# Kernel tuning notes

Hardware: AMD Instinct MI355X
Metric: run time of the kernel (lower is better)

The kernel has to match this reference:

```python
import jax, jax.numpy as jnp
import numpy as np

H_DIM = 1024
N_HEADS = 16
HEAD_D = H_DIM // N_HEADS  # 64


def setup_inputs() -> dict:
    key = jax.random.key(0)
    ks = jax.random.split(key, 10)
    B, T, C = 2, 2048, H_DIM
    init = 1.0 / np.sqrt(C)  # lecun_normal-scale stand-in
    src = jax.random.normal(ks[0], (B, T, C), dtype=jnp.float32)
    mask = jnp.ones((B, T), dtype=jnp.float32)  # unused when causal
    Wq = jax.random.normal(ks[1], (C, H_DIM), dtype=jnp.float32) * init
    Wk = jax.random.normal(ks[2], (C, H_DIM), dtype=jnp.float32) * init
    Wv = jax.random.normal(ks[3], (C, H_DIM), dtype=jnp.float32) * init
    Wo = jax.random.normal(ks[4], (H_DIM, H_DIM), dtype=jnp.float32) * init
    bq = jnp.zeros((H_DIM,), jnp.float32)
    bk = jnp.zeros((H_DIM,), jnp.float32)
    bv = jnp.zeros((H_DIM,), jnp.float32)
    bo = jnp.zeros((H_DIM,), jnp.float32)
    return {"src": src, "mask": mask, "Wq": Wq, "bq": bq, "Wk": Wk, "bk": bk,
            "Wv": Wv, "bv": bv, "Wo": Wo, "bo": bo}


def reference(src, mask, Wq, bq, Wk, bk, Wv, bv, Wo, bo):
    # MaskedCausalAttention forward, deterministic=True (dropout = identity),
    # use_causal_mask=True.
    B, T, C = src.shape
    N, D = N_HEADS, HEAD_D
    # q,k,v: [B, N, T, D]
    q = (src @ Wq + bq).reshape(B, T, N, D).transpose(0, 2, 1, 3)
    k = (src @ Wk + bk).reshape(B, T, N, D).transpose(0, 2, 1, 3)
    v = (src @ Wv + bv).reshape(B, T, N, D).transpose(0, 2, 1, 3)
    # scores: [B, N, T, T]
    scores = jnp.einsum('bntd,bnsd->bnts', q, k) / jnp.sqrt(jnp.float32(D))
    causal = jnp.tril(jnp.ones((T, T), dtype=bool))[None, None]
    scores = jnp.where(causal, scores, -jnp.inf)
    probs = jax.nn.softmax(scores, axis=-1)
    attn = jnp.einsum('bnts,bnsd->bntd', probs, v)  # [B, N, T, D]
    attn = attn.transpose(0, 2, 1, 3).reshape(B, T, N * D)
    return attn @ Wo + bo
```

## Files before the change

kernel.cpp:

```cpp
#include <hip/hip_runtime.h>
#include <hip/hip_bf16.h>

typedef __hip_bfloat16 bf16;
typedef __attribute__((ext_vector_type(8))) short short8;
typedef __attribute__((ext_vector_type(4))) float f32x4;

#define BATCH 2
#define SEQ   2048
#define HDIM  1024
#define NHEAD 16
#define DHEAD 64
#define MROWS (BATCH*SEQ)

#define QSCALE 0.18033688f
#define EXP2F(x) __builtin_amdgcn_exp2f(x)

static __device__ __forceinline__ short f2bs(float x) {
    __hip_bfloat16 h = (__hip_bfloat16)x;
    return *reinterpret_cast<short*>(&h);
}
static __device__ __forceinline__ unsigned int pk2(float a, float b) {
    __hip_bfloat162 h = __float22bfloat162_rn(make_float2(a, b));
    return *reinterpret_cast<unsigned int*>(&h);
}

static __device__ __forceinline__ void gload16(const void* g, void* l) {
    __builtin_amdgcn_global_load_lds(
        (const __attribute__((address_space(1))) unsigned int*)g,
        (__attribute__((address_space(3))) unsigned int*)l, 16, 0, 0);
}

__global__ __launch_bounds__(256) void prep1(const float* __restrict__ src,
        const float* __restrict__ Wq, const float* __restrict__ Wk,
        const float* __restrict__ Wv, const float* __restrict__ Wo,
        short* __restrict__ Sb, short* __restrict__ WT,
        short* __restrict__ WoT)
{
    __shared__ float t[64][65];
    const int bx = blockIdx.x, tid = threadIdx.x;
    if (bx < 4096) {
        int i = bx * 256 + tid;
        float4 v = ((const float4*)src)[i];
        ushort4 o;
        o.x = (unsigned short)f2bs(v.x);
        o.y = (unsigned short)f2bs(v.y);
        o.z = (unsigned short)f2bs(v.z);
        o.w = (unsigned short)f2bs(v.w);
        ((ushort4*)Sb)[i] = o;
        return;
    }
    const int tb = bx - 4096;
    const int wsel = tb >> 8;
    const float* W = (wsel == 0) ? Wq : (wsel == 1) ? Wk : (wsel == 2) ? Wv : Wo;
    short* dst = (wsel < 3) ? WT : WoT;
    const int roff = (wsel < 3) ? wsel * 1024 : 0;
    const int t8 = tb & 255;
    const int n0 = (t8 & 15) * 64, k0 = (t8 >> 4) * 64;
#pragma unroll
    for (int i = 0; i < 16; i++) {
        int idx = tid + i * 256, r = idx >> 6, c = idx & 63;
        t[r][c] = W[(size_t)(k0 + r) * HDIM + n0 + c];
    }
    __syncthreads();
#pragma unroll
    for (int i = 0; i < 16; i++) {
        int idx = tid + i * 256, c = idx >> 6, r = idx & 63;
        dst[(size_t)(roff + n0 + c) * HDIM + k0 + r] = f2bs(t[r][c]);
    }
}

__global__ __launch_bounds__(512, 2) void gemm_qkv(const short* __restrict__ A,
        const short* __restrict__ Bt,
        const float* __restrict__ bq, const float* __restrict__ bk,
        const float* __restrict__ bv,
        short* __restrict__ Qout, short* __restrict__ Kout,
        short* __restrict__ Vtout)
{
    __shared__ short SM[2 * 12288];
    const int tid = threadIdx.x, lane = tid & 63, w = tid >> 6;
    const int quad = lane >> 4, l15 = lane & 15;
    const int m0 = blockIdx.y * 256, n0 = blockIdx.x * 128;
    const int wr = w >> 1, wc = w & 1;

    const short* gsrc[3];
    short* ldst[3];
#pragma unroll
    for (int i = 0; i < 3; i++) {
        int u = w * 3 + i;
        if (u < 16) {
            gsrc[i] = A + (size_t)(m0 + u * 16 + l15) * HDIM + quad * 8;
            ldst[i] = &SM[u * 512];
        } else {
            int v = u - 16;
            gsrc[i] = Bt + (size_t)(n0 + v * 16 + l15) * HDIM + quad * 8;
            ldst[i] = &SM[8192 + v * 512];
        }
    }

    f32x4 acc[4][4];
#pragma unroll
    for (int i = 0; i < 4; i++)
#pragma unroll
        for (int j = 0; j < 4; j++) acc[i][j] = (f32x4){0.f, 0.f, 0.f, 0.f};

#pragma unroll
    for (int i = 0; i < 3; i++) { gload16(gsrc[i], ldst[i]); gsrc[i] += 32; }

    for (int kk = 0; kk < 32; ++kk) {
        const int cur = kk & 1;
        if (kk < 31) {
            const int nb = (cur ^ 1) * 12288;
#pragma unroll
            for (int i = 0; i < 3; i++) { gload16(gsrc[i], ldst[i] + nb); gsrc[i] += 32; }
            asm volatile("s_waitcnt vmcnt(3)" ::: "memory");
        } else {
            asm volatile("s_waitcnt vmcnt(0)" ::: "memory");
        }
        __builtin_amdgcn_s_barrier();
        const short* Asb = &SM[cur * 12288];
        const short* Bsb = Asb + 8192;
        short8 af[4], bfr[4];
#pragma unroll
        for (int mi = 0; mi < 4; mi++)
            af[mi] = *(const short8*)&Asb[(wr * 4 + mi) * 512 + lane * 8];
#pragma unroll
        for (int ni = 0; ni < 4; ni++)
            bfr[ni] = *(const short8*)&Bsb[(wc * 4 + ni) * 512 + lane * 8];
#pragma unroll
        for (int mi = 0; mi < 4; mi++)
#pragma unroll
            for (int ni = 0; ni < 4; ni++)
                acc[mi][ni] = __builtin_amdgcn_mfma_f32_16x16x32_bf16(
                                  af[mi], bfr[ni], acc[mi][ni], 0, 0, 0);
        __builtin_amdgcn_s_barrier();
    }

    const int region = n0 >> 10;
    if (region < 2) {
        const float* bias = region ? bk : bq;
        const float oscale = region ? 1.0f : QSCALE;
        short* C = region ? Kout : Qout;
#pragma unroll
        for (int mi = 0; mi < 4; mi++) {
            int mB = m0 + (wr * 4 + mi) * 16 + quad * 4;
#pragma unroll
            for (int ni = 0; ni < 4; ni++) {
                int nl = (n0 + (wc * 4 + ni) * 16 + l15) & 1023;
                float bb = bias[nl];
#pragma unroll
                for (int r = 0; r < 4; r++)
                    C[(size_t)(mB + r) * HDIM + nl] =
                        f2bs((acc[mi][ni][r] + bb) * oscale);
            }
        }
    } else {
#pragma unroll
        for (int mi = 0; mi < 4; mi++) {
            int mB = m0 + (wr * 4 + mi) * 16 + quad * 4;
            int bb = mB >> 11, t = mB & 2047;
#pragma unroll
            for (int ni = 0; ni < 4; ni++) {
                int n = n0 + (wc * 4 + ni) * 16 + l15;
                int h = (n >> 6) & 15, d = n & 63;
                float bvv = bv[n & 1023];
                size_t base = ((size_t)((bb * NHEAD + h) * DHEAD + d)) * SEQ + t;
                ushort4 pk;
                pk.x = (unsigned short)f2bs(acc[mi][ni][0] + bvv);
                pk.y = (unsigned short)f2bs(acc[mi][ni][1] + bvv);
                pk.z = (unsigned short)f2bs(acc[mi][ni][2] + bvv);
                pk.w = (unsigned short)f2bs(acc[mi][ni][3] + bvv);
                *(ushort4*)(Vtout + base) = pk;
            }
        }
    }
}

__global__ __launch_bounds__(256) void attn_mfma(const short* __restrict__ Qb,
        const short* __restrict__ Kb, const short* __restrict__ Vt,
        short* __restrict__ Ab)
{
    __shared__ short SMEM[20992];
    const int tid = threadIdx.x, lane = tid & 63, w = tid >> 6;
    const int quad = lane >> 4, l15 = lane & 15;
    const int L = blockIdx.x;

    const int pair = (L & 7) + 8 * ((L >> 3) & 3);
    const int strip = 31 - (L >> 5);
    const int b = pair >> 4, head = pair & 15;

    const short* Kbh = Kb + (size_t)b * SEQ * HDIM + head * DHEAD;
    const short* Vth = Vt + (size_t)(b * NHEAD + head) * DHEAD * SEQ;
    short* Pw = SMEM + 16384 + w * 1152;

    const int qbase = strip * 64;
    const int qr = qbase + w * 16 + l15;

    const short* qptr = Qb + (size_t)(b * SEQ + qr) * HDIM + head * DHEAD + quad * 8;
    short8 bq0 = *(const short8*)qptr;
    short8 bq1 = *(const short8*)(qptr + 32);

    const short* gp[4];
    int stp[4], ldo[4];
#pragma unroll
    for (int i = 0; i < 4; i++) {
        int u = w * 4 + i;
        if (u < 8) {
            int t = u >> 1, h = u & 1;
            gp[i] = Kbh + (size_t)(t * 16 + l15) * HDIM + h * 32 + quad * 8;
            stp[i] = 64 * HDIM;
        } else {
            int c = u - 8, dt = c >> 1, kh = c & 1;
            gp[i] = Vth + (size_t)(dt * 16 + l15) * SEQ + kh * 32 + quad * 8;
            stp[i] = 64;
        }
        ldo[i] = u * 512;
    }

    f32x4 o[4];
#pragma unroll
    for (int dt = 0; dt < 4; dt++) o[dt] = (f32x4){0.f, 0.f, 0.f, 0.f};
    float psum = 0.f;

#pragma unroll
    for (int i = 0; i < 4; i++) { gload16(gp[i], &SMEM[ldo[i]]); gp[i] += stp[i]; }

    for (int it = 0; it <= strip; ++it) {
        const int cur = it & 1;
        short* Ks = &SMEM[cur * 8192];
        short* Vs = Ks + 4096;

        if (it < strip) {
            short* nb = &SMEM[(cur ^ 1) * 8192];
#pragma unroll
            for (int i = 0; i < 4; i++) { gload16(gp[i], nb + ldo[i]); gp[i] += stp[i]; }
            asm volatile("s_waitcnt vmcnt(4)" ::: "memory");
        } else {
            asm volatile("s_waitcnt vmcnt(0)" ::: "memory");
        }
        __builtin_amdgcn_s_barrier();
        const int s0 = it * 64;
        f32x4 sv[4];
        __builtin_amdgcn_s_setprio(1);
#pragma unroll
        for (int t = 0; t < 4; t++) {
            sv[t] = (f32x4){0.f, 0.f, 0.f, 0.f};
            short8 k0 = *(const short8*)&Ks[(t * 2) * 512 + lane * 8];
            short8 k1 = *(const short8*)&Ks[(t * 2 + 1) * 512 + lane * 8];
            sv[t] = __builtin_amdgcn_mfma_f32_16x16x32_bf16(k0, bq0, sv[t], 0, 0, 0);
            sv[t] = __builtin_amdgcn_mfma_f32_16x16x32_bf16(k1, bq1, sv[t], 0, 0, 0);
        }
        __builtin_amdgcn_s_setprio(0);

        float p[16];
        if (it == strip) {
#pragma unroll
            for (int t = 0; t < 4; t++)
#pragma unroll
                for (int r = 0; r < 4; r++) {
                    int key = s0 + t * 16 + quad * 4 + r;
                    p[t * 4 + r] = (key <= qr) ? EXP2F(sv[t][r]) : 0.f;
                }
        } else {
#pragma unroll
            for (int t = 0; t < 4; t++)
#pragma unroll
                for (int r = 0; r < 4; r++)
                    p[t * 4 + r] = EXP2F(sv[t][r]);
        }
#pragma unroll
        for (int i = 0; i < 16; i++) psum += p[i];

#pragma unroll
        for (int t = 0; t < 4; t++) {
            uint2 u2;
            u2.x = pk2(p[t * 4],     p[t * 4 + 1]);
            u2.y = pk2(p[t * 4 + 2], p[t * 4 + 3]);
            *(uint2*)&Pw[l15 * 72 + t * 16 + quad * 4] = u2;
        }
        short8 bp0 = *(const short8*)&Pw[l15 * 72 + quad * 8];
        short8 bp1 = *(const short8*)&Pw[l15 * 72 + 32 + quad * 8];

        __builtin_amdgcn_s_setprio(1);
#pragma unroll
        for (int dt = 0; dt < 4; dt++) {
            short8 av0 = *(const short8*)&Vs[(dt * 2) * 512 + lane * 8];
            short8 av1 = *(const short8*)&Vs[(dt * 2 + 1) * 512 + lane * 8];
            o[dt] = __builtin_amdgcn_mfma_f32_16x16x32_bf16(av0, bp0, o[dt], 0, 0, 0);
            o[dt] = __builtin_amdgcn_mfma_f32_16x16x32_bf16(av1, bp1, o[dt], 0, 0, 0);
        }
        __builtin_amdgcn_s_setprio(0);
        __builtin_amdgcn_s_barrier();
    }

    float lrow = psum + __shfl_xor(psum, 16);
    lrow += __shfl_xor(lrow, 32);
    const float inv = 1.f / lrow;

    const size_t obase = (size_t)(b * SEQ + qr) * HDIM + head * DHEAD;
#pragma unroll
    for (int dt = 0; dt < 4; dt++) {
        uint2 u2;
        u2.x = pk2(o[dt][0] * inv, o[dt][1] * inv);
        u2.y = pk2(o[dt][2] * inv, o[dt][3] * inv);
        *(uint2*)&Ab[obase + dt * 16 + quad * 4] = u2;
    }
}

__global__ __launch_bounds__(256) void gemm_o(const short* __restrict__ A,
        const short* __restrict__ Bt, const float* __restrict__ bo,
        float* __restrict__ Out)
{
    __shared__ short SM[2 * 6144];
    const int tid = threadIdx.x, lane = tid & 63, w = tid >> 6;
    const int quad = lane >> 4, l15 = lane & 15;
    const int m0 = blockIdx.y * 64, n0 = blockIdx.x * 128;
    const int wr = w >> 1, wc = w & 1;

    const short* gsrc[3];
    short* ldst[3];
#pragma unroll
    for (int i = 0; i < 3; i++) {
        int u = w * 3 + i;
        if (u < 4) {
            gsrc[i] = A + (size_t)(m0 + u * 16 + l15) * HDIM + quad * 8;
            ldst[i] = &SM[u * 512];
        } else {
            int v = u - 4;
            gsrc[i] = Bt + (size_t)(n0 + v * 16 + l15) * HDIM + quad * 8;
            ldst[i] = &SM[2048 + v * 512];
        }
    }

    f32x4 acc[2][4];
#pragma unroll
    for (int i = 0; i < 2; i++)
#pragma unroll
        for (int j = 0; j < 4; j++) acc[i][j] = (f32x4){0.f, 0.f, 0.f, 0.f};

#pragma unroll
    for (int i = 0; i < 3; i++) { gload16(gsrc[i], ldst[i]); gsrc[i] += 32; }

    for (int kk = 0; kk < 32; ++kk) {
        const int cur = kk & 1;
        if (kk < 31) {
            const int nb = (cur ^ 1) * 6144;
#pragma unroll
            for (int i = 0; i < 3; i++) { gload16(gsrc[i], ldst[i] + nb); gsrc[i] += 32; }
            asm volatile("s_waitcnt vmcnt(3)" ::: "memory");
        } else {
            asm volatile("s_waitcnt vmcnt(0)" ::: "memory");
        }
        __builtin_amdgcn_s_barrier();

        const short* Asb = &SM[cur * 6144];
        const short* Bsb = Asb + 2048;
        short8 af[2], bfr[4];
#pragma unroll
        for (int mi = 0; mi < 2; mi++)
            af[mi] = *(const short8*)&Asb[(wr * 2 + mi) * 512 + lane * 8];
#pragma unroll
        for (int ni = 0; ni < 4; ni++)
            bfr[ni] = *(const short8*)&Bsb[(wc * 4 + ni) * 512 + lane * 8];
#pragma unroll
        for (int mi = 0; mi < 2; mi++)
#pragma unroll
            for (int ni = 0; ni < 4; ni++)
                acc[mi][ni] = __builtin_amdgcn_mfma_f32_16x16x32_bf16(
                                  af[mi], bfr[ni], acc[mi][ni], 0, 0, 0);
        __builtin_amdgcn_s_barrier();
    }

#pragma unroll
    for (int mi = 0; mi < 2; mi++) {
        int mB = m0 + (wr * 2 + mi) * 16 + quad * 4;
#pragma unroll
        for (int ni = 0; ni < 4; ni++) {
            int n = n0 + (wc * 4 + ni) * 16 + l15;
            float bb = bo[n];
#pragma unroll
            for (int r = 0; r < 4; r++)
                Out[(size_t)(mB + r) * HDIM + n] = acc[mi][ni][r] + bb;
        }
    }
}

extern "C" void kernel_launch(void* const* d_in, const int* in_sizes, int n_in,
                              void* d_out, int out_size, void* d_ws, size_t ws_size,
                              hipStream_t stream)
{
    const float* src = (const float*)d_in[0];
    const float* Wq = (const float*)d_in[2];
    const float* bq = (const float*)d_in[3];
    const float* Wk = (const float*)d_in[4];
    const float* bk = (const float*)d_in[5];
    const float* Wv = (const float*)d_in[6];
    const float* bv = (const float*)d_in[7];
    const float* Wo = (const float*)d_in[8];
    const float* bo = (const float*)d_in[9];
    float* out = (float*)d_out;

    short* Sb   = (short*)d_ws;
    short* Qb   = Sb + (size_t)MROWS * HDIM;
    short* Kb   = Qb + (size_t)MROWS * HDIM;
    short* Vt   = Kb + (size_t)MROWS * HDIM;
    short* WoT  = Vt + (size_t)MROWS * HDIM;
    short* WT   = (short*)d_out;
    short* Ab   = Qb;

    prep1<<<dim3(4096 + 1024), dim3(256), 0, stream>>>(src, Wq, Wk, Wv, Wo, Sb, WT, WoT);

    gemm_qkv<<<dim3(24, 16), dim3(512), 0, stream>>>(Sb, WT, bq, bk, bv, Qb, Kb, Vt);

    attn_mfma<<<dim3(1024), dim3(256), 0, stream>>>(Qb, Kb, Vt, Ab);

    gemm_o<<<dim3(8, 64), dim3(256), 0, stream>>>(Ab, WoT, bo, out);
}
```

Measured before the change: 210.5 us.

## Triple-buffer LDS tiles in QKV, attention and output GEMM kernels

Replaces double-buffered global-to-LDS staging with a three-stage ring buffer in all three MFMA kernels, issuing loads two iterations ahead and relaxing the vmcnt waits to match. This hides more global-memory latency behind the MFMA work. The cost is more LDS per block (QKV GEMM grows to 72KB), which may lower occupancy, and modulo-3 indexing adds a little integer work.

```diff
diff --git a/kernel.cpp b/kernel.cpp
--- a/kernel.cpp
+++ b/kernel.cpp
@@ -76,7 +76,7 @@
         short* __restrict__ Qout, short* __restrict__ Kout,
         short* __restrict__ Vtout)
 {
-    __shared__ short SM[2 * 12288];
+    __shared__ short SM[3 * 12288];
     const int tid = threadIdx.x, lane = tid & 63, w = tid >> 6;
     const int quad = lane >> 4, l15 = lane & 15;
     const int m0 = blockIdx.y * 256, n0 = blockIdx.x * 128;
@@ -105,19 +105,22 @@
 
 #pragma unroll
     for (int i = 0; i < 3; i++) { gload16(gsrc[i], ldst[i]); gsrc[i] += 32; }
+#pragma unroll
+    for (int i = 0; i < 3; i++) { gload16(gsrc[i], ldst[i] + 12288); gsrc[i] += 32; }
 
     for (int kk = 0; kk < 32; ++kk) {
-        const int cur = kk & 1;
-        if (kk < 31) {
-            const int nb = (cur ^ 1) * 12288;
+        if (kk < 30) {
+            const int nb = ((kk + 2) % 3) * 12288;
 #pragma unroll
             for (int i = 0; i < 3; i++) { gload16(gsrc[i], ldst[i] + nb); gsrc[i] += 32; }
+            asm volatile("s_waitcnt vmcnt(6)" ::: "memory");
+        } else if (kk == 30) {
             asm volatile("s_waitcnt vmcnt(3)" ::: "memory");
         } else {
             asm volatile("s_waitcnt vmcnt(0)" ::: "memory");
         }
         __builtin_amdgcn_s_barrier();
-        const short* Asb = &SM[cur * 12288];
+        const short* Asb = &SM[(kk % 3) * 12288];
         const short* Bsb = Asb + 8192;
         short8 af[4], bfr[4];
 #pragma unroll
@@ -179,7 +182,7 @@
         const short* __restrict__ Kb, const short* __restrict__ Vt,
         short* __restrict__ Ab)
 {
-    __shared__ short SMEM[20992];
+    __shared__ short SMEM[29184];
     const int tid = threadIdx.x, lane = tid & 63, w = tid >> 6;
     const int quad = lane >> 4, l15 = lane & 15;
     const int L = blockIdx.x;
@@ -190,7 +193,7 @@
 
     const short* Kbh = Kb + (size_t)b * SEQ * HDIM + head * DHEAD;
     const short* Vth = Vt + (size_t)(b * NHEAD + head) * DHEAD * SEQ;
-    short* Pw = SMEM + 16384 + w * 1152;
+    short* Pw = SMEM + 24576 + w * 1152;
 
     const int qbase = strip * 64;
     const int qr = qbase + w * 16 + l15;
@@ -223,16 +226,21 @@
 
 #pragma unroll
     for (int i = 0; i < 4; i++) { gload16(gp[i], &SMEM[ldo[i]]); gp[i] += stp[i]; }
+    if (strip >= 1) {
+#pragma unroll
+        for (int i = 0; i < 4; i++) { gload16(gp[i], &SMEM[8192 + ldo[i]]); gp[i] += stp[i]; }
+    }
 
     for (int it = 0; it <= strip; ++it) {
-        const int cur = it & 1;
-        short* Ks = &SMEM[cur * 8192];
+        short* Ks = &SMEM[(it % 3) * 8192];
         short* Vs = Ks + 4096;
 
-        if (it < strip) {
-            short* nb = &SMEM[(cur ^ 1) * 8192];
+        if (it + 2 <= strip) {
+            short* nb = &SMEM[((it + 2) % 3) * 8192];
 #pragma unroll
             for (int i = 0; i < 4; i++) { gload16(gp[i], nb + ldo[i]); gp[i] += stp[i]; }
+            asm volatile("s_waitcnt vmcnt(8)" ::: "memory");
+        } else if (it + 1 <= strip) {
             asm volatile("s_waitcnt vmcnt(4)" ::: "memory");
         } else {
             asm volatile("s_waitcnt vmcnt(0)" ::: "memory");
@@ -310,7 +318,7 @@
         const short* __restrict__ Bt, const float* __restrict__ bo,
         float* __restrict__ Out)
 {
-    __shared__ short SM[2 * 6144];
+    __shared__ short SM[3 * 6144];
     const int tid = threadIdx.x, lane = tid & 63, w = tid >> 6;
     const int quad = lane >> 4, l15 = lane & 15;
     const int m0 = blockIdx.y * 64, n0 = blockIdx.x * 128;
@@ -339,20 +347,23 @@
 
 #pragma unroll
     for (int i = 0; i < 3; i++) { gload16(gsrc[i], ldst[i]); gsrc[i] += 32; }
+#pragma unroll
+    for (int i = 0; i < 3; i++) { gload16(gsrc[i], ldst[i] + 6144); gsrc[i] += 32; }
 
     for (int kk = 0; kk < 32; ++kk) {
-        const int cur = kk & 1;
-        if (kk < 31) {
-            const int nb = (cur ^ 1) * 6144;
+        if (kk < 30) {
+            const int nb = ((kk + 2) % 3) * 6144;
 #pragma unroll
             for (int i = 0; i < 3; i++) { gload16(gsrc[i], ldst[i] + nb); gsrc[i] += 32; }
+            asm volatile("s_waitcnt vmcnt(6)" ::: "memory");
+        } else if (kk == 30) {
             asm volatile("s_waitcnt vmcnt(3)" ::: "memory");
         } else {
             asm volatile("s_waitcnt vmcnt(0)" ::: "memory");
         }
         __builtin_amdgcn_s_barrier();
 
-        const short* Asb = &SM[cur * 6144];
+        const short* Asb = &SM[(kk % 3) * 6144];
         const short* Bsb = Asb + 2048;
         short8 af[2], bfr[4];
 #pragma unroll
```

Measured after the change: 212.3 us. About the same (+0.9%).
